# Performance work log

Hardware: AMD Instinct MI355X
Metric: run time of the kernel (lower is better)

The kernel has to match this reference:

```python
import jax, jax.numpy as jnp
import numpy as np

B, T, C, H = 16, 2048, 1024, 64

def setup_inputs() -> dict:
    key = jax.random.key(0)
    kx, kq, kk, kv = jax.random.split(key, 4)
    x = jax.random.normal(kx, (B, T, C), dtype=jnp.float32)
    Wq = jax.random.normal(kq, (C, H), dtype=jnp.float32) * (C ** -0.5)
    Wk = jax.random.normal(kk, (C, H), dtype=jnp.float32) * (C ** -0.5)
    Wv = jax.random.normal(kv, (C, H), dtype=jnp.float32) * (C ** -0.5)
    return {"x": x, "Wq": Wq, "Wk": Wk, "Wv": Wv}

def reference(x, Wq, Wk, Wv):
    # q,k,v: [B,T,H]
    q = jnp.einsum('btc,ch->bth', x, Wq)
    k = jnp.einsum('btc,ch->bth', x, Wk)
    v = jnp.einsum('btc,ch->bth', x, Wv)
    scale = k.shape[-1] ** -0.5
    # scores: [B,T,T], causal mask then softmax (dropout=0 -> identity)
    w = jnp.einsum('bth,bsh->bts', q, k) * scale
    causal = jnp.tril(jnp.ones((x.shape[1], x.shape[1]), dtype=bool))
    w = jnp.where(causal[None, :, :], w, -jnp.inf)
    w = jax.nn.softmax(w, axis=-1)
    out = jnp.einsum('bts,bsh->bth', w, v)
    return out
```

## Files before the change

### kernel.cpp

```cpp
#include <hip/hip_runtime.h>


#define B_ 16
#define T_ 2048
#define C_ 1024
#define H_ 64
#define QK_ELEMS (B_ * T_ * H_)

typedef float  f32x4  __attribute__((ext_vector_type(4)));
typedef __bf16 bf16x8 __attribute__((ext_vector_type(8)));
typedef __bf16 bf16x4 __attribute__((ext_vector_type(4)));

__device__ __forceinline__ void glds16(const void* g, void* l) {
    __builtin_amdgcn_global_load_lds(
        (const __attribute__((address_space(1))) void*)g,
        (__attribute__((address_space(3))) void*)l, 16, 0, 0);
}

__global__ __launch_bounds__(256) void wt_kernel(const float* __restrict__ Wq,
                                                 const float* __restrict__ Wk,
                                                 const float* __restrict__ Wv,
                                                 __bf16* __restrict__ Wt) {
    __shared__ float tl[64][65];
    const int mat = blockIdx.x >> 4;
    const int c0  = (blockIdx.x & 15) * 64;
    const float* W = (mat == 0) ? Wq : (mat == 1) ? Wk : Wv;
    const int t  = threadIdx.x;
    const int r4 = t >> 6;
    const int cc = t & 63;
#pragma unroll
    for (int i = 0; i < 16; i++) {
        const int c = r4 + i * 4;
        tl[c][cc] = W[(size_t)(c0 + c) * H_ + cc];
    }
    __syncthreads();
#pragma unroll
    for (int i = 0; i < 16; i++) {
        const int h = r4 + i * 4;
        const int cc2 = ((((cc >> 3) ^ (h & 7)) << 3) | (cc & 7));
        Wt[(size_t)mat * 65536 + (size_t)h * C_ + c0 + cc2] = (__bf16)tl[cc][h];
    }
}

__global__ __launch_bounds__(256) void qkv_kernel(const float* __restrict__ x,
                                                  const __bf16* __restrict__ Wt,
                                                  __bf16* __restrict__ Qw,
                                                  __bf16* __restrict__ Kw,
                                                  __bf16* __restrict__ Vtw) {
    __shared__ __align__(16) __bf16 Blds[3][192 * 64];

    const int tid  = threadIdx.x;
    const int w    = tid >> 6;
    const int lane = tid & 63;
    const int quad = lane >> 4;
    const int l15  = lane & 15;
    const int wm   = (w & 1) * 32;
    const int wn   = (w >> 1) * 96;
    const int m0   = blockIdx.x * 64;

    f32x4 acc[12];
#pragma unroll
    for (int i = 0; i < 12; i++) acc[i] = (f32x4){0.f, 0.f, 0.f, 0.f};

    const float* xA0 = x + (size_t)(m0 + wm + l15) * C_ + quad * 8;
    const float* xA1 = xA0 + 16 * C_;

    float4 a0[8], a1[8];
    auto loadA = [&](float4 (&as)[8], int k0) {
#pragma unroll
        for (int kh = 0; kh < 2; kh++) {
            as[kh * 4 + 0] = *(const float4*)(xA0 + k0 + kh * 32);
            as[kh * 4 + 1] = *(const float4*)(xA0 + k0 + kh * 32 + 4);
            as[kh * 4 + 2] = *(const float4*)(xA1 + k0 + kh * 32);
            as[kh * 4 + 3] = *(const float4*)(xA1 + k0 + kh * 32 + 4);
        }
    };

    const __bf16* bsrc = Wt + (size_t)(w * 48 + (lane >> 3)) * C_ + (lane & 7) * 8;
    auto stageB = [&](int k0, int buf) {
        __bf16* dst = &Blds[buf][(w * 48) * 64];
        const __bf16* src = bsrc + k0;
#pragma unroll
        for (int i = 0; i < 6; i++)
            glds16(src + (size_t)i * 8 * C_, dst + i * 8 * 64);
    };

    auto step = [&](float4 (&as)[8], int k) {
        __asm__ __volatile__("s_waitcnt vmcnt(14)" ::: "memory");
        __builtin_amdgcn_s_barrier();
        const int kn = (k + 2 <= 15) ? k + 2 : 15;
        stageB(kn * 64, (k + 2) % 3);

        bf16x8 af[2][2];
#pragma unroll
        for (int kh = 0; kh < 2; kh++)
#pragma unroll
            for (int mt = 0; mt < 2; mt++) {
                const float4 p = as[kh * 4 + mt * 2 + 0];
                const float4 q = as[kh * 4 + mt * 2 + 1];
                bf16x8 v;
                v[0]=(__bf16)p.x; v[1]=(__bf16)p.y; v[2]=(__bf16)p.z; v[3]=(__bf16)p.w;
                v[4]=(__bf16)q.x; v[5]=(__bf16)q.y; v[6]=(__bf16)q.z; v[7]=(__bf16)q.w;
                af[mt][kh] = v;
            }
        loadA(as, kn * 64);

        const int buf = k % 3;
#pragma unroll
        for (int kh = 0; kh < 2; kh++) {
            const int ch8 = ((((kh << 2) + quad) ^ (l15 & 7)) << 3);
#pragma unroll
            for (int nt = 0; nt < 6; nt++) {
                bf16x8 bfr = *(const bf16x8*)&Blds[buf][(wn + nt * 16 + l15) * 64 + ch8];
                acc[nt]     = __builtin_amdgcn_mfma_f32_16x16x32_bf16(af[0][kh], bfr, acc[nt], 0, 0, 0);
                acc[6 + nt] = __builtin_amdgcn_mfma_f32_16x16x32_bf16(af[1][kh], bfr, acc[6 + nt], 0, 0, 0);
            }
        }
    };

    stageB(0, 0);  loadA(a0, 0);
    stageB(64, 1); loadA(a1, 64);

    for (int k = 0; k < 16; k += 2) {
        step(a0, k);
        step(a1, k + 1);
    }

    __asm__ __volatile__("s_waitcnt vmcnt(0)" ::: "memory");
    __syncthreads();

#pragma unroll
    for (int mt = 0; mt < 2; mt++) {
        const int row0 = m0 + wm + mt * 16 + quad * 4;
#pragma unroll
        for (int nt = 0; nt < 6; nt++) {
            const int col = wn + nt * 16 + l15;
            const f32x4 acv = acc[mt * 6 + nt];
            if (wn + nt * 16 < 64) {
#pragma unroll
                for (int r = 0; r < 4; r++)
                    Qw[(size_t)(row0 + r) * H_ + col] = (__bf16)acv[r];
            } else if (wn + nt * 16 < 128) {
                const int h = col - 64;
#pragma unroll
                for (int r = 0; r < 4; r++) {
                    const int row = row0 + r;
                    const int hs  = (((h >> 3) ^ (row & 7)) << 3) | (h & 7);
                    Kw[(size_t)row * H_ + hs] = (__bf16)acv[r];
                }
            }
        }
    }
    __bf16* Vt_l = &Blds[0][0];
    if (w >= 2) {
#pragma unroll
        for (int mt = 0; mt < 2; mt++) {
            const int t0 = wm + mt * 16 + quad * 4;
#pragma unroll
            for (int nt = 2; nt < 6; nt++) {
                const int h = (nt - 2) * 16 + l15;
                const f32x4 acv = acc[mt * 6 + nt];
                bf16x4 pv;
                pv[0]=(__bf16)acv[0]; pv[1]=(__bf16)acv[1];
                pv[2]=(__bf16)acv[2]; pv[3]=(__bf16)acv[3];
                *(bf16x4*)&Vt_l[h * 72 + t0] = pv;
            }
        }
    }
    __syncthreads();
    if (w >= 2) {
        const int bb   = m0 >> 11;
        const int tblk = m0 & 2047;
#pragma unroll
        for (int i = 0; i < 4; i++) {
            const int hh = (w - 2) * 32 + i * 8 + (lane >> 3);
            const int cs = (((lane & 7) ^ (lane >> 3)) << 3);
            *(bf16x8*)(Vtw + (((size_t)(bb * H_ + hh)) << 11) + tblk + ((lane & 7) << 3)) =
                *(const bf16x8*)&Vt_l[hh * 72 + cs];
        }
    }
}

#define SCALE_LOG2E 0.18033688011112042f

__global__ __launch_bounds__(256) void attn_kernel(const __bf16* __restrict__ Qw,
                                                   const __bf16* __restrict__ Kw,
                                                   const __bf16* __restrict__ Vtw,
                                                   float* __restrict__ Opart,
                                                   float* __restrict__ Lpart) {
    __shared__ __align__(16) __bf16 Klds[2][64 * 64];
    __shared__ __align__(16) __bf16 Vlds[2][64 * 64];
    __shared__ __align__(16) __bf16 Plds[2][4][16 * 72];

    const int tid  = threadIdx.x;
    const int w    = tid >> 6;
    const int lane = tid & 63;
    const int quad = lane >> 4;
    const int l15  = lane & 15;

    const int b   = blockIdx.x & 15;
    const int cid = blockIdx.x >> 4;
    int i, ci;
    if (cid < 16)      { i = 15 - (cid >> 2); ci = cid & 3; }
    else if (cid < 28) { const int u = cid - 16; i = 11 - u / 3; ci = u % 3; }
    else if (cid < 36) { const int u = cid - 28; i = 7 - (u >> 1); ci = u & 1; }
    else               { i = 3 - (cid - 36); ci = 0; }

    const int jmax = 2 * i + 1;
    const int j0 = ci * 8;
    const int j1 = (j0 + 8 < jmax + 1) ? j0 + 8 : jmax + 1;
    const int nj = j1 - j0;
    const int qA0 = 2 * i * 64;
    const size_t bT = (size_t)b * T_;

    const __bf16* qpA = Qw + (bT + qA0 + w * 16 + l15) * H_ + quad * 8;
    const bf16x8 qfA0 = *(const bf16x8*)qpA;
    const bf16x8 qfA1 = *(const bf16x8*)(qpA + 32);
    const bf16x8 qfB0 = *(const bf16x8*)(qpA + 64 * H_);
    const bf16x8 qfB1 = *(const bf16x8*)(qpA + 64 * H_ + 32);

    float lA = 0.f, lB = 0.f;
    f32x4 accA[4], accB[4];
#pragma unroll
    for (int nt = 0; nt < 4; nt++) {
        accA[nt] = (f32x4){0.f, 0.f, 0.f, 0.f};
        accB[nt] = (f32x4){0.f, 0.f, 0.f, 0.f};
    }

    auto stage = [&](int ts0, int buf) {
        const __bf16* Ks = Kw + (bT + ts0) * H_;
        const __bf16* Vs = Vtw + (((size_t)(b * H_)) << 11) + ts0;
#pragma unroll
        for (int c = 0; c < 2; c++) {
            const int g   = w * 2 + c;
            const int row = g * 8 + (lane >> 3);
            const int cb  = (lane & 7) * 8;
            glds16(Ks + (size_t)row * H_ + cb, &Klds[buf][g * 512]);
            glds16(Vs + ((size_t)row << 11) + cb, &Vlds[buf][g * 512]);
        }
    };

    stage(j0 * 64, 0);

    for (int jj = 0; jj < nj; jj++) {
        const int j = j0 + jj;
        __syncthreads();
        if (jj + 1 < nj) stage((j + 1) * 64, (jj + 1) & 1);
        const int buf = jj & 1;
        const bool doA = (j <= 2 * i);
        const int ts0 = j * 64;
        const int qgA = qA0 + w * 16 + l15;

#pragma unroll
        for (int nt = 0; nt < 4; nt++) {
            const __bf16* kb = &Klds[buf][(nt * 16 + l15) * 64];
            bf16x8 kf0 = *(const bf16x8*)(kb + ((quad ^ (l15 & 7)) << 3));
            bf16x8 kf1 = *(const bf16x8*)(kb + (((4 + quad) ^ (l15 & 7)) << 3));
            const int key0 = ts0 + nt * 16 + quad * 4;

            if (doA) {
                f32x4 z = (f32x4){0.f, 0.f, 0.f, 0.f};
                z = __builtin_amdgcn_mfma_f32_16x16x32_bf16(kf0, qfA0, z, 0, 0, 0);
                z = __builtin_amdgcn_mfma_f32_16x16x32_bf16(kf1, qfA1, z, 0, 0, 0);
                bf16x4 pv;
#pragma unroll
                for (int r = 0; r < 4; r++) {
                    float e = exp2f(__builtin_fmaf(z[r], SCALE_LOG2E, -8.0f));
                    if (j == 2 * i && key0 + r > qgA) e = 0.f;
                    pv[r] = (__bf16)e;
                    lA += e;
                }
                *(bf16x4*)&Plds[0][w][l15 * 72 + nt * 16 + quad * 4] = pv;
            }
            {
                f32x4 z = (f32x4){0.f, 0.f, 0.f, 0.f};
                z = __builtin_amdgcn_mfma_f32_16x16x32_bf16(kf0, qfB0, z, 0, 0, 0);
                z = __builtin_amdgcn_mfma_f32_16x16x32_bf16(kf1, qfB1, z, 0, 0, 0);
                bf16x4 pv;
#pragma unroll
                for (int r = 0; r < 4; r++) {
                    float e = exp2f(__builtin_fmaf(z[r], SCALE_LOG2E, -8.0f));
                    if (j == jmax && key0 + r > qgA + 64) e = 0.f;
                    pv[r] = (__bf16)e;
                    lB += e;
                }
                *(bf16x4*)&Plds[1][w][l15 * 72 + nt * 16 + quad * 4] = pv;
            }
        }
        __asm__ __volatile__("s_waitcnt lgkmcnt(0)" ::: "memory");

        const __bf16* prA = &Plds[0][w][l15 * 72];
        const __bf16* prB = &Plds[1][w][l15 * 72];
        bf16x8 pfA0, pfA1;
        if (doA) {
            pfA0 = *(const bf16x8*)(prA + quad * 8);
            pfA1 = *(const bf16x8*)(prA + 32 + quad * 8);
        }
        bf16x8 pfB0 = *(const bf16x8*)(prB + quad * 8);
        bf16x8 pfB1 = *(const bf16x8*)(prB + 32 + quad * 8);
#pragma unroll
        for (int nt = 0; nt < 4; nt++) {
            const __bf16* vb = &Vlds[buf][(nt * 16 + l15) * 64];
            bf16x8 vf0 = *(const bf16x8*)(vb + ((quad ^ (l15 & 7)) << 3));
            bf16x8 vf1 = *(const bf16x8*)(vb + (((4 + quad) ^ (l15 & 7)) << 3));
            if (doA) {
                accA[nt] = __builtin_amdgcn_mfma_f32_16x16x32_bf16(pfA0, vf0, accA[nt], 0, 0, 0);
                accA[nt] = __builtin_amdgcn_mfma_f32_16x16x32_bf16(pfA1, vf1, accA[nt], 0, 0, 0);
            }
            accB[nt] = __builtin_amdgcn_mfma_f32_16x16x32_bf16(pfB0, vf0, accB[nt], 0, 0, 0);
            accB[nt] = __builtin_amdgcn_mfma_f32_16x16x32_bf16(pfB1, vf1, accB[nt], 0, 0, 0);
        }
    }

    lA += __shfl_xor(lA, 16); lA += __shfl_xor(lA, 32);
    lB += __shfl_xor(lB, 16); lB += __shfl_xor(lB, 32);

    const int qiA = 2 * i;
    const int slotA = ((((b << 5) + qiA) << 2) + ci);
    const int slotB = ((((b << 5) + qiA + 1) << 2) + ci);
    float* OpA = Opart + (size_t)slotA * 4096;
    float* OpB = Opart + (size_t)slotB * 4096;
#pragma unroll
    for (int nt = 0; nt < 4; nt++)
#pragma unroll
        for (int r = 0; r < 4; r++) {
            const int o = (w * 16 + quad * 4 + r) * 64 + nt * 16 + l15;
            OpA[o] = accA[nt][r];
            OpB[o] = accB[nt][r];
        }
    if (quad == 0) {
        Lpart[slotA * 64 + w * 16 + l15] = lA;
        Lpart[slotB * 64 + w * 16 + l15] = lB;
    }
}

__global__ __launch_bounds__(256) void reduce_kernel(const float* __restrict__ Opart,
                                                     const float* __restrict__ Lpart,
                                                     float* __restrict__ out) {
    const int b  = blockIdx.x & 15;
    const int qi = blockIdx.x >> 4;
    const int nc = ((qi & ~1) + 9) >> 3;
    const int tid = threadIdx.x;
    const int q  = tid >> 2;
    const int hc = (tid & 3) * 16;
    const int sbase = ((b << 5) + qi) << 2;

    f32x4 s[4];
#pragma unroll
    for (int i = 0; i < 4; i++) s[i] = (f32x4){0.f, 0.f, 0.f, 0.f};
    float l = 0.f;
    for (int ci = 0; ci < nc; ci++) {
        const float* Op = Opart + (size_t)(sbase + ci) * 4096 + q * 64 + hc;
#pragma unroll
        for (int i = 0; i < 4; i++) s[i] += *(const f32x4*)(Op + i * 4);
        l += Lpart[(sbase + ci) * 64 + q];
    }
    const float inv = 1.f / l;
    float* o = out + ((size_t)b * T_ + qi * 64 + q) * H_ + hc;
#pragma unroll
    for (int i = 0; i < 4; i++) {
        f32x4 r = s[i] * inv;
        *(f32x4*)(o + i * 4) = r;
    }
}

extern "C" void kernel_launch(void* const* d_in, const int* in_sizes, int n_in,
                              void* d_out, int out_size, void* d_ws, size_t ws_size,
                              hipStream_t stream) {
    const float* x  = (const float*)d_in[0];
    const float* Wq = (const float*)d_in[1];
    const float* Wk = (const float*)d_in[2];
    const float* Wv = (const float*)d_in[3];
    float* out = (float*)d_out;

    __bf16* Qw  = (__bf16*)d_ws;
    __bf16* Kw  = Qw + QK_ELEMS;
    __bf16* Vtw = Kw + QK_ELEMS;
    __bf16* Wt  = Vtw + QK_ELEMS;
    float* Opart = (float*)((char*)d_ws + 16777216);
    float* Lpart = Opart + (size_t)2048 * 4096;

    wt_kernel<<<dim3(48), dim3(256), 0, stream>>>(Wq, Wk, Wv, Wt);
    qkv_kernel<<<dim3((B_ * T_) / 64), dim3(256), 0, stream>>>(x, Wt, Qw, Kw, Vtw);
    attn_kernel<<<dim3(640), dim3(256), 0, stream>>>(Qw, Kw, Vtw, Opart, Lpart);
    reduce_kernel<<<dim3(512), dim3(256), 0, stream>>>(Opart, Lpart, out);
}
```

Measured before the change: 285.4 us.

## Load QKV weight fragments directly into registers instead of staging via LDS

The QKV projection kernel no longer stages weight tiles through a triple-buffered LDS ring with global_load_lds and barriers. Each wave now loads its B fragments straight from global memory into double-buffered registers, and the kernel gains a launch bound of 2 blocks per CU. This removes the per-step barriers and the LDS traffic, and shrinks shared memory to the V transpose buffer only. The cost is much higher register pressure (24 bf16x8 B fragments plus the A prefetch) and duplicated global/L2 reads of the weights, since the two waves that share a column range each load it.

```diff
diff --git a/kernel.cpp b/kernel.cpp
--- a/kernel.cpp
+++ b/kernel.cpp
@@ -42,12 +42,12 @@
     }
 }
 
-__global__ __launch_bounds__(256) void qkv_kernel(const float* __restrict__ x,
-                                                  const __bf16* __restrict__ Wt,
-                                                  __bf16* __restrict__ Qw,
-                                                  __bf16* __restrict__ Kw,
-                                                  __bf16* __restrict__ Vtw) {
-    __shared__ __align__(16) __bf16 Blds[3][192 * 64];
+__global__ __launch_bounds__(256, 2) void qkv_kernel(const float* __restrict__ x,
+                                                     const __bf16* __restrict__ Wt,
+                                                     __bf16* __restrict__ Qw,
+                                                     __bf16* __restrict__ Kw,
+                                                     __bf16* __restrict__ Vtw) {
+    __shared__ __align__(16) __bf16 Vt_l[64 * 72];
 
     const int tid  = threadIdx.x;
     const int w    = tid >> 6;
@@ -64,8 +64,13 @@
 
     const float* xA0 = x + (size_t)(m0 + wm + l15) * C_ + quad * 8;
     const float* xA1 = xA0 + 16 * C_;
+    const __bf16* bB = Wt + (size_t)(wn + l15) * C_;
+    const int ch8a = ((quad ^ (l15 & 7)) << 3);
+    const int ch8b = (((4 + quad) ^ (l15 & 7)) << 3);
 
     float4 a0[8], a1[8];
+    bf16x8 b0[12], b1[12];
+
     auto loadA = [&](float4 (&as)[8], int k0) {
 #pragma unroll
         for (int kh = 0; kh < 2; kh++) {
@@ -75,22 +80,16 @@
             as[kh * 4 + 3] = *(const float4*)(xA1 + k0 + kh * 32 + 4);
         }
     };
-
-    const __bf16* bsrc = Wt + (size_t)(w * 48 + (lane >> 3)) * C_ + (lane & 7) * 8;
-    auto stageB = [&](int k0, int buf) {
-        __bf16* dst = &Blds[buf][(w * 48) * 64];
-        const __bf16* src = bsrc + k0;
-#pragma unroll
-        for (int i = 0; i < 6; i++)
-            glds16(src + (size_t)i * 8 * C_, dst + i * 8 * 64);
+    auto loadB = [&](bf16x8 (&bs)[12], int k) {
+        const __bf16* bk = bB + k * 64;
+#pragma unroll
+        for (int nt = 0; nt < 6; nt++) {
+            bs[nt * 2 + 0] = *(const bf16x8*)(bk + (size_t)nt * 16 * C_ + ch8a);
+            bs[nt * 2 + 1] = *(const bf16x8*)(bk + (size_t)nt * 16 * C_ + ch8b);
+        }
     };
 
-    auto step = [&](float4 (&as)[8], int k) {
-        __asm__ __volatile__("s_waitcnt vmcnt(14)" ::: "memory");
-        __builtin_amdgcn_s_barrier();
-        const int kn = (k + 2 <= 15) ? k + 2 : 15;
-        stageB(kn * 64, (k + 2) % 3);
-
+    auto step = [&](float4 (&as)[8], bf16x8 (&bs)[12], int k) {
         bf16x8 af[2][2];
 #pragma unroll
         for (int kh = 0; kh < 2; kh++)
@@ -103,31 +102,24 @@
                 v[4]=(__bf16)q.x; v[5]=(__bf16)q.y; v[6]=(__bf16)q.z; v[7]=(__bf16)q.w;
                 af[mt][kh] = v;
             }
-        loadA(as, kn * 64);
-
-        const int buf = k % 3;
-#pragma unroll
-        for (int kh = 0; kh < 2; kh++) {
-            const int ch8 = ((((kh << 2) + quad) ^ (l15 & 7)) << 3);
+        if (k + 2 < 16) loadA(as, (k + 2) * 64);
+#pragma unroll
+        for (int kh = 0; kh < 2; kh++)
 #pragma unroll
             for (int nt = 0; nt < 6; nt++) {
-                bf16x8 bfr = *(const bf16x8*)&Blds[buf][(wn + nt * 16 + l15) * 64 + ch8];
-                acc[nt]     = __builtin_amdgcn_mfma_f32_16x16x32_bf16(af[0][kh], bfr, acc[nt], 0, 0, 0);
-                acc[6 + nt] = __builtin_amdgcn_mfma_f32_16x16x32_bf16(af[1][kh], bfr, acc[6 + nt], 0, 0, 0);
-            }
-        }
+                acc[nt]     = __builtin_amdgcn_mfma_f32_16x16x32_bf16(af[0][kh], bs[nt * 2 + kh], acc[nt], 0, 0, 0);
+                acc[6 + nt] = __builtin_amdgcn_mfma_f32_16x16x32_bf16(af[1][kh], bs[nt * 2 + kh], acc[6 + nt], 0, 0, 0);
+            }
+        if (k + 2 < 16) loadB(bs, k + 2);
     };
 
-    stageB(0, 0);  loadA(a0, 0);
-    stageB(64, 1); loadA(a1, 64);
+    loadA(a0, 0);  loadB(b0, 0);
+    loadA(a1, 64); loadB(b1, 1);
 
     for (int k = 0; k < 16; k += 2) {
-        step(a0, k);
-        step(a1, k + 1);
-    }
-
-    __asm__ __volatile__("s_waitcnt vmcnt(0)" ::: "memory");
-    __syncthreads();
+        step(a0, b0, k);
+        step(a1, b1, k + 1);
+    }
 
 #pragma unroll
     for (int mt = 0; mt < 2; mt++) {
@@ -151,7 +143,6 @@
             }
         }
     }
-    __bf16* Vt_l = &Blds[0][0];
     if (w >= 2) {
 #pragma unroll
         for (int mt = 0; mt < 2; mt++) {
```

Result: slower. 308.1 us (+8.0%).
